# Kernel tuning notes

Measured on AMD Instinct MI355X. Metric: run time of the kernel, lower is better.

The kernel has to match this reference:

```python
import jax, jax.numpy as jnp
import numpy as np

B, H, S, D = 2, 16, 2048, 64

def setup_inputs() -> dict:
    key = jax.random.key(0)
    kq, kk, kv = jax.random.split(key, 3)
    q = jax.random.normal(kq, (B, H, S, D), dtype=jnp.float32)
    k = jax.random.normal(kk, (B, H, S, D), dtype=jnp.float32)
    v = jax.random.normal(kv, (B, H, S, D), dtype=jnp.float32)
    # causal mask: True where position j > i (future tokens are masked)
    mask = jnp.triu(jnp.ones((S, S), dtype=bool), k=1)[None, None, :, :]
    return {"q": q, "k": k, "v": v, "mask": mask}

def reference(q, k, v, mask) -> jnp.ndarray:
    # scaled dot-product attention with additive -1e4 mask bias
    scale = 1.0 / jnp.sqrt(jnp.asarray(q.shape[-1], q.dtype))
    scores = jnp.einsum('bhqd,bhkd->bhqk', q, k) * scale  # [B,H,S,S]
    scores = scores + mask.astype(scores.dtype) * jnp.asarray(-10000.0, scores.dtype)
    probs = jax.nn.softmax(scores, axis=-1)
    # dropout is identity in eval mode
    return jnp.einsum('bhqk,bhkd->bhqd', probs, v)
```

## Files before the change

### kernel.cpp

```cpp
#include <hip/hip_runtime.h>

typedef __bf16 bf16_t;
typedef bf16_t bf16x8 __attribute__((ext_vector_type(8)));
typedef bf16_t bf16x4 __attribute__((ext_vector_type(4)));
typedef float  floatx4 __attribute__((ext_vector_type(4)));

constexpr int Sq = 2048, Dq = 64;
constexpr int BQ = 64, BK = 64;
constexpr int NQT = Sq / BQ;
constexpr int STR = 72;
constexpr float SCALE_LOG2E = 0.125f * 1.44269504088896340736f;

__global__ __launch_bounds__(256, 2) void flash_attn_kernel(
    const float* __restrict__ Q, const float* __restrict__ K,
    const float* __restrict__ V, float* __restrict__ O)
{
    __shared__ bf16_t QPs[BQ][STR];
    __shared__ bf16_t Ks[BK][STR];
    __shared__ bf16_t VTs[Dq][STR];

    const int tid  = threadIdx.x;
    const int wave = tid >> 6;
    const int lane = tid & 63;
    const int quad = lane >> 4;
    const int l16  = lane & 15;

    const int id = blockIdx.x;
    const int bh = (id & 7) + ((id >> 7) << 3);
    const int pr = (id >> 3) & 15;
    const long base = (long)bh * Sq * Dq;

    const int r0 = tid >> 4;
    const int c4 = (tid & 15) * 4;
    const int h  = lane >> 3;
    const int jw = wave * 16;

    for (int half = 0; half < 2; ++half) {
        const int qt = half ? (NQT - 1 - pr) : pr;

        __syncthreads();
        #pragma unroll
        for (int p = 0; p < 4; ++p) {
            const int row = p * 16 + r0;
            const float4 qv = *(const float4*)&Q[base + (long)(qt * BQ + row) * Dq + c4];
            bf16x4 w;
            w[0] = (bf16_t)(qv.x * SCALE_LOG2E); w[1] = (bf16_t)(qv.y * SCALE_LOG2E);
            w[2] = (bf16_t)(qv.z * SCALE_LOG2E); w[3] = (bf16_t)(qv.w * SCALE_LOG2E);
            *(bf16x4*)&QPs[row][c4] = w;
        }
        __syncthreads();

        bf16x8 aq0, aq1;
        {
            const int qrow = wave * 16 + l16;
            aq0 = *(const bf16x8*)&QPs[qrow][quad * 8];
            aq1 = *(const bf16x8*)&QPs[qrow][32 + quad * 8];
        }

        float l_lane = 0.f;
        floatx4 o_acc[4];
        #pragma unroll
        for (int i = 0; i < 4; ++i) o_acc[i] = floatx4{0.f, 0.f, 0.f, 0.f};

        float4 kf[4];
        float  vf[4][4];
        #pragma unroll
        for (int p = 0; p < 4; ++p) {
            kf[p] = *(const float4*)&K[base + (long)(p * 16 + r0) * Dq + c4];
            const int j0 = jw + 4 * ((p + h) & 3);
            #pragma unroll
            for (int r = 0; r < 4; ++r)
                vf[p][r] = V[base + (long)(j0 + r) * Dq + lane];
        }

        for (int kt = 0; kt <= qt; ++kt) {
            __syncthreads();

            #pragma unroll
            for (int p = 0; p < 4; ++p) {
                bf16x4 w;
                w[0] = (bf16_t)kf[p].x; w[1] = (bf16_t)kf[p].y;
                w[2] = (bf16_t)kf[p].z; w[3] = (bf16_t)kf[p].w;
                *(bf16x4*)&Ks[p * 16 + r0][c4] = w;
                bf16x4 vw;
                vw[0] = (bf16_t)vf[p][0]; vw[1] = (bf16_t)vf[p][1];
                vw[2] = (bf16_t)vf[p][2]; vw[3] = (bf16_t)vf[p][3];
                *(bf16x4*)&VTs[lane][jw + 4 * ((p + h) & 3)] = vw;
            }
            __syncthreads();

            {
                const int kn = (kt < qt) ? (kt + 1) : qt;
                const long kb = base + (long)kn * BK * Dq;
                #pragma unroll
                for (int p = 0; p < 4; ++p) {
                    kf[p] = *(const float4*)&K[kb + (long)(p * 16 + r0) * Dq + c4];
                    const int j0 = jw + 4 * ((p + h) & 3);
                    #pragma unroll
                    for (int r = 0; r < 4; ++r)
                        vf[p][r] = V[kb + (long)(j0 + r) * Dq + lane];
                }
            }

            floatx4 acc[4];
            #pragma unroll
            for (int t = 0; t < 4; ++t) {
                acc[t] = floatx4{0.f, 0.f, 0.f, 0.f};
                const int krow = t * 16 + l16;
                bf16x8 ak0 = *(const bf16x8*)&Ks[krow][quad * 8];
                bf16x8 ak1 = *(const bf16x8*)&Ks[krow][32 + quad * 8];
                acc[t] = __builtin_amdgcn_mfma_f32_16x16x32_bf16(ak0, aq0, acc[t], 0, 0, 0);
                acc[t] = __builtin_amdgcn_mfma_f32_16x16x32_bf16(ak1, aq1, acc[t], 0, 0, 0);
            }

            if (kt == qt) {
                const int qr = wave * 16 + l16;
                #pragma unroll
                for (int t = 0; t < 4; ++t) {
                    #pragma unroll
                    for (int i = 0; i < 4; ++i) {
                        if (t * 16 + quad * 4 + i > qr) acc[t][i] = -1e30f;
                    }
                }
            }

            float l_add = 0.f;
            #pragma unroll
            for (int t = 0; t < 4; ++t) {
                #pragma unroll
                for (int i = 0; i < 4; ++i) {
                    acc[t][i] = __builtin_amdgcn_exp2f(acc[t][i]);
                    l_add += acc[t][i];
                }
            }
            l_lane += l_add;

            #pragma unroll
            for (int t = 0; t < 4; ++t) {
                bf16x4 pk;
                pk[0] = (bf16_t)acc[t][0]; pk[1] = (bf16_t)acc[t][1];
                pk[2] = (bf16_t)acc[t][2]; pk[3] = (bf16_t)acc[t][3];
                *(bf16x4*)&QPs[wave * 16 + l16][t * 16 + quad * 4] = pk;
            }

            bf16x8 ap0 = *(const bf16x8*)&QPs[wave * 16 + l16][quad * 8];
            bf16x8 ap1 = *(const bf16x8*)&QPs[wave * 16 + l16][32 + quad * 8];
            #pragma unroll
            for (int dt = 0; dt < 4; ++dt) {
                const int dcol = dt * 16 + l16;
                bf16x8 bv0 = *(const bf16x8*)&VTs[dcol][quad * 8];
                bf16x8 bv1 = *(const bf16x8*)&VTs[dcol][32 + quad * 8];
                o_acc[dt] = __builtin_amdgcn_mfma_f32_16x16x32_bf16(ap0, bv0, o_acc[dt], 0, 0, 0);
                o_acc[dt] = __builtin_amdgcn_mfma_f32_16x16x32_bf16(ap1, bv1, o_acc[dt], 0, 0, 0);
            }
        }

        float lsum = l_lane;
        lsum += __shfl_xor(lsum, 16);
        lsum += __shfl_xor(lsum, 32);
        #pragma unroll
        for (int i = 0; i < 4; ++i) {
            const float inv_l = 1.f / __shfl(lsum, quad * 4 + i, 16);
            const long row = (long)qt * BQ + wave * 16 + quad * 4 + i;
            #pragma unroll
            for (int dt = 0; dt < 4; ++dt) {
                O[base + row * Dq + dt * 16 + l16] = o_acc[dt][i] * inv_l;
            }
        }
    }
}

extern "C" void kernel_launch(void* const* d_in, const int* in_sizes, int n_in,
                              void* d_out, int out_size, void* d_ws, size_t ws_size,
                              hipStream_t stream)
{
    const float* q = (const float*)d_in[0];
    const float* k = (const float*)d_in[1];
    const float* v = (const float*)d_in[2];
    float* out = (float*)d_out;
    flash_attn_kernel<<<dim3(512, 1, 1), dim3(256, 1, 1), 0, stream>>>(q, k, v, out);
}
```

Before: 128.3 us.

## Double-buffer K/V shared tiles to drop one barrier per iteration

Splits the K and transposed-V shared tiles into two buffers. Each iteration writes the next tile into the spare buffer while computing on the current one, so only one barrier per iteration is needed instead of two. Register prefetch now runs two tiles ahead. Shared memory use grows by about 18 KB per block, which may limit occupancy at two blocks per CU.

```diff
diff --git a/kernel.cpp b/kernel.cpp
--- a/kernel.cpp
+++ b/kernel.cpp
@@ -16,8 +16,8 @@
     const float* __restrict__ V, float* __restrict__ O)
 {
     __shared__ bf16_t QPs[BQ][STR];
-    __shared__ bf16_t Ks[BK][STR];
-    __shared__ bf16_t VTs[Dq][STR];
+    __shared__ bf16_t Ks[2][BK][STR];
+    __shared__ bf16_t VTs[2][Dq][STR];
 
     const int tid  = threadIdx.x;
     const int wave = tid >> 6;
@@ -72,26 +72,49 @@
             for (int r = 0; r < 4; ++r)
                 vf[p][r] = V[base + (long)(j0 + r) * Dq + lane];
         }
+        #pragma unroll
+        for (int p = 0; p < 4; ++p) {
+            bf16x4 w;
+            w[0] = (bf16_t)kf[p].x; w[1] = (bf16_t)kf[p].y;
+            w[2] = (bf16_t)kf[p].z; w[3] = (bf16_t)kf[p].w;
+            *(bf16x4*)&Ks[0][p * 16 + r0][c4] = w;
+            bf16x4 vw;
+            vw[0] = (bf16_t)vf[p][0]; vw[1] = (bf16_t)vf[p][1];
+            vw[2] = (bf16_t)vf[p][2]; vw[3] = (bf16_t)vf[p][3];
+            *(bf16x4*)&VTs[0][lane][jw + 4 * ((p + h) & 3)] = vw;
+        }
+        {
+            const int kn = (qt > 0) ? 1 : 0;
+            const long kb = base + (long)kn * BK * Dq;
+            #pragma unroll
+            for (int p = 0; p < 4; ++p) {
+                kf[p] = *(const float4*)&K[kb + (long)(p * 16 + r0) * Dq + c4];
+                const int j0 = jw + 4 * ((p + h) & 3);
+                #pragma unroll
+                for (int r = 0; r < 4; ++r)
+                    vf[p][r] = V[kb + (long)(j0 + r) * Dq + lane];
+            }
+        }
+        __syncthreads();
 
         for (int kt = 0; kt <= qt; ++kt) {
-            __syncthreads();
-
-            #pragma unroll
-            for (int p = 0; p < 4; ++p) {
-                bf16x4 w;
-                w[0] = (bf16_t)kf[p].x; w[1] = (bf16_t)kf[p].y;
-                w[2] = (bf16_t)kf[p].z; w[3] = (bf16_t)kf[p].w;
-                *(bf16x4*)&Ks[p * 16 + r0][c4] = w;
-                bf16x4 vw;
-                vw[0] = (bf16_t)vf[p][0]; vw[1] = (bf16_t)vf[p][1];
-                vw[2] = (bf16_t)vf[p][2]; vw[3] = (bf16_t)vf[p][3];
-                *(bf16x4*)&VTs[lane][jw + 4 * ((p + h) & 3)] = vw;
-            }
-            __syncthreads();
-
-            {
-                const int kn = (kt < qt) ? (kt + 1) : qt;
-                const long kb = base + (long)kn * BK * Dq;
+            const int cur = kt & 1;
+
+            if (kt < qt) {
+                #pragma unroll
+                for (int p = 0; p < 4; ++p) {
+                    bf16x4 w;
+                    w[0] = (bf16_t)kf[p].x; w[1] = (bf16_t)kf[p].y;
+                    w[2] = (bf16_t)kf[p].z; w[3] = (bf16_t)kf[p].w;
+                    *(bf16x4*)&Ks[cur ^ 1][p * 16 + r0][c4] = w;
+                    bf16x4 vw;
+                    vw[0] = (bf16_t)vf[p][0]; vw[1] = (bf16_t)vf[p][1];
+                    vw[2] = (bf16_t)vf[p][2]; vw[3] = (bf16_t)vf[p][3];
+                    *(bf16x4*)&VTs[cur ^ 1][lane][jw + 4 * ((p + h) & 3)] = vw;
+                }
+            }
+            if (kt + 1 < qt) {
+                const long kb = base + (long)(kt + 2) * BK * Dq;
                 #pragma unroll
                 for (int p = 0; p < 4; ++p) {
                     kf[p] = *(const float4*)&K[kb + (long)(p * 16 + r0) * Dq + c4];
@@ -107,8 +130,8 @@
             for (int t = 0; t < 4; ++t) {
                 acc[t] = floatx4{0.f, 0.f, 0.f, 0.f};
                 const int krow = t * 16 + l16;
-                bf16x8 ak0 = *(const bf16x8*)&Ks[krow][quad * 8];
-                bf16x8 ak1 = *(const bf16x8*)&Ks[krow][32 + quad * 8];
+                bf16x8 ak0 = *(const bf16x8*)&Ks[cur][krow][quad * 8];
+                bf16x8 ak1 = *(const bf16x8*)&Ks[cur][krow][32 + quad * 8];
                 acc[t] = __builtin_amdgcn_mfma_f32_16x16x32_bf16(ak0, aq0, acc[t], 0, 0, 0);
                 acc[t] = __builtin_amdgcn_mfma_f32_16x16x32_bf16(ak1, aq1, acc[t], 0, 0, 0);
             }
@@ -148,11 +171,13 @@
             #pragma unroll
             for (int dt = 0; dt < 4; ++dt) {
                 const int dcol = dt * 16 + l16;
-                bf16x8 bv0 = *(const bf16x8*)&VTs[dcol][quad * 8];
-                bf16x8 bv1 = *(const bf16x8*)&VTs[dcol][32 + quad * 8];
+                bf16x8 bv0 = *(const bf16x8*)&VTs[cur][dcol][quad * 8];
+                bf16x8 bv1 = *(const bf16x8*)&VTs[cur][dcol][32 + quad * 8];
                 o_acc[dt] = __builtin_amdgcn_mfma_f32_16x16x32_bf16(ap0, bv0, o_acc[dt], 0, 0, 0);
                 o_acc[dt] = __builtin_amdgcn_mfma_f32_16x16x32_bf16(ap1, bv1, o_acc[dt], 0, 0, 0);
             }
+
+            __syncthreads();
         }
 
         float lsum = l_lane;
```

Result: slower. 134.2 us (+4.6%).

## Enlarge query tile to 128 rows per block, drop paired-tile scheduling

Applied to the files above, without the earlier changes.

The query tile grows from 64 to 128 rows, so each wave computes two 16-row query sub-tiles against every staged K/V tile. This halves K/V global loads, bf16 conversions and LDS staging per query row. The old scheme, where each block processed a light and a heavy 64-row tile for causal balance, is replaced by a single 128-row tile per block, with block-index remapping that interleaves ascending and descending tile order. Blocks now do very different amounts of causal work (2 to 32 key tiles), so load imbalance and a longer critical path are a risk.

```diff
diff --git a/kernel.cpp b/kernel.cpp
--- a/kernel.cpp
+++ b/kernel.cpp
@@ -6,7 +6,7 @@
 typedef float  floatx4 __attribute__((ext_vector_type(4)));
 
 constexpr int Sq = 2048, Dq = 64;
-constexpr int BQ = 64, BK = 64;
+constexpr int BQ = 128, BK = 64;
 constexpr int NQT = Sq / BQ;
 constexpr int STR = 72;
 constexpr float SCALE_LOG2E = 0.125f * 1.44269504088896340736f;
@@ -25,9 +25,12 @@
     const int quad = lane >> 4;
     const int l16  = lane & 15;
 
-    const int id = blockIdx.x;
-    const int bh = (id & 7) + ((id >> 7) << 3);
-    const int pr = (id >> 3) & 15;
+    const int b  = blockIdx.x;
+    const int x  = b & 255;
+    const int bh = (x & 7) | (((x >> 7) & 1) << 3) | (((b >> 8) & 1) << 4);
+    const int qidx = (x >> 3) & 15;
+    const int qt = (b >> 8) ? (NQT - 1 - qidx) : qidx;
+    const int ktmax = 2 * qt + 1;
     const long base = (long)bh * Sq * Dq;
 
     const int r0 = tid >> 4;
@@ -35,136 +38,157 @@
     const int h  = lane >> 3;
     const int jw = wave * 16;
 
-    for (int half = 0; half < 2; ++half) {
-        const int qt = half ? (NQT - 1 - pr) : pr;
-
+    #pragma unroll
+    for (int p = 0; p < 8; ++p) {
+        const int row = p * 16 + r0;
+        const float4 qv = *(const float4*)&Q[base + (long)(qt * BQ + row) * Dq + c4];
+        bf16x4 w;
+        w[0] = (bf16_t)(qv.x * SCALE_LOG2E); w[1] = (bf16_t)(qv.y * SCALE_LOG2E);
+        w[2] = (bf16_t)(qv.z * SCALE_LOG2E); w[3] = (bf16_t)(qv.w * SCALE_LOG2E);
+        *(bf16x4*)&QPs[row][c4] = w;
+    }
+    __syncthreads();
+
+    bf16x8 aq[2][2];
+    #pragma unroll
+    for (int u = 0; u < 2; ++u) {
+        #pragma unroll
+        for (int hh = 0; hh < 2; ++hh)
+            aq[u][hh] = *(const bf16x8*)&QPs[32 * wave + u * 16 + l16][hh * 32 + quad * 8];
+    }
+
+    float l_lane[2] = {0.f, 0.f};
+    floatx4 o_acc[2][4];
+    #pragma unroll
+    for (int u = 0; u < 2; ++u)
+        #pragma unroll
+        for (int dt = 0; dt < 4; ++dt) o_acc[u][dt] = floatx4{0.f, 0.f, 0.f, 0.f};
+
+    float4 kf[4];
+    float  vf[4][4];
+    #pragma unroll
+    for (int p = 0; p < 4; ++p) {
+        kf[p] = *(const float4*)&K[base + (long)(p * 16 + r0) * Dq + c4];
+        const int j0 = jw + 4 * ((p + h) & 3);
+        #pragma unroll
+        for (int r = 0; r < 4; ++r)
+            vf[p][r] = V[base + (long)(j0 + r) * Dq + lane];
+    }
+
+    for (int kt = 0; kt <= ktmax; ++kt) {
         __syncthreads();
+
         #pragma unroll
         for (int p = 0; p < 4; ++p) {
-            const int row = p * 16 + r0;
-            const float4 qv = *(const float4*)&Q[base + (long)(qt * BQ + row) * Dq + c4];
             bf16x4 w;
-            w[0] = (bf16_t)(qv.x * SCALE_LOG2E); w[1] = (bf16_t)(qv.y * SCALE_LOG2E);
-            w[2] = (bf16_t)(qv.z * SCALE_LOG2E); w[3] = (bf16_t)(qv.w * SCALE_LOG2E);
-            *(bf16x4*)&QPs[row][c4] = w;
+            w[0] = (bf16_t)kf[p].x; w[1] = (bf16_t)kf[p].y;
+            w[2] = (bf16_t)kf[p].z; w[3] = (bf16_t)kf[p].w;
+            *(bf16x4*)&Ks[p * 16 + r0][c4] = w;
+            bf16x4 vw;
+            vw[0] = (bf16_t)vf[p][0]; vw[1] = (bf16_t)vf[p][1];
+            vw[2] = (bf16_t)vf[p][2]; vw[3] = (bf16_t)vf[p][3];
+            *(bf16x4*)&VTs[lane][jw + 4 * ((p + h) & 3)] = vw;
         }
         __syncthreads();
 
-        bf16x8 aq0, aq1;
         {
-            const int qrow = wave * 16 + l16;
-            aq0 = *(const bf16x8*)&QPs[qrow][quad * 8];
-            aq1 = *(const bf16x8*)&QPs[qrow][32 + quad * 8];
-        }
-
-        float l_lane = 0.f;
-        floatx4 o_acc[4];
-        #pragma unroll
-        for (int i = 0; i < 4; ++i) o_acc[i] = floatx4{0.f, 0.f, 0.f, 0.f};
-
-        float4 kf[4];
-        float  vf[4][4];
-        #pragma unroll
-        for (int p = 0; p < 4; ++p) {
-            kf[p] = *(const float4*)&K[base + (long)(p * 16 + r0) * Dq + c4];
-            const int j0 = jw + 4 * ((p + h) & 3);
-            #pragma unroll
-            for (int r = 0; r < 4; ++r)
-                vf[p][r] = V[base + (long)(j0 + r) * Dq + lane];
-        }
-
-        for (int kt = 0; kt <= qt; ++kt) {
-            __syncthreads();
-
+            const int kn = (kt < ktmax) ? (kt + 1) : ktmax;
+            const long kb = base + (long)kn * BK * Dq;
             #pragma unroll
             for (int p = 0; p < 4; ++p) {
-                bf16x4 w;
-                w[0] = (bf16_t)kf[p].x; w[1] = (bf16_t)kf[p].y;
-                w[2] = (bf16_t)kf[p].z; w[3] = (bf16_t)kf[p].w;
-                *(bf16x4*)&Ks[p * 16 + r0][c4] = w;
-                bf16x4 vw;
-                vw[0] = (bf16_t)vf[p][0]; vw[1] = (bf16_t)vf[p][1];
-                vw[2] = (bf16_t)vf[p][2]; vw[3] = (bf16_t)vf[p][3];
-                *(bf16x4*)&VTs[lane][jw + 4 * ((p + h) & 3)] = vw;
-            }
-            __syncthreads();
-
-            {
-                const int kn = (kt < qt) ? (kt + 1) : qt;
-                const long kb = base + (long)kn * BK * Dq;
+                kf[p] = *(const float4*)&K[kb + (long)(p * 16 + r0) * Dq + c4];
+                const int j0 = jw + 4 * ((p + h) & 3);
                 #pragma unroll
-                for (int p = 0; p < 4; ++p) {
-                    kf[p] = *(const float4*)&K[kb + (long)(p * 16 + r0) * Dq + c4];
-                    const int j0 = jw + 4 * ((p + h) & 3);
-                    #pragma unroll
-                    for (int r = 0; r < 4; ++r)
-                        vf[p][r] = V[kb + (long)(j0 + r) * Dq + lane];
-                }
-            }
-
-            floatx4 acc[4];
-            #pragma unroll
-            for (int t = 0; t < 4; ++t) {
-                acc[t] = floatx4{0.f, 0.f, 0.f, 0.f};
-                const int krow = t * 16 + l16;
-                bf16x8 ak0 = *(const bf16x8*)&Ks[krow][quad * 8];
-                bf16x8 ak1 = *(const bf16x8*)&Ks[krow][32 + quad * 8];
-                acc[t] = __builtin_amdgcn_mfma_f32_16x16x32_bf16(ak0, aq0, acc[t], 0, 0, 0);
-                acc[t] = __builtin_amdgcn_mfma_f32_16x16x32_bf16(ak1, aq1, acc[t], 0, 0, 0);
-            }
-
-            if (kt == qt) {
-                const int qr = wave * 16 + l16;
+                for (int r = 0; r < 4; ++r)
+                    vf[p][r] = V[kb + (long)(j0 + r) * Dq + lane];
+            }
+        }
+
+        floatx4 acc[4][2];
+        #pragma unroll
+        for (int t = 0; t < 4; ++t) {
+            const int krow = t * 16 + l16;
+            bf16x8 ak0 = *(const bf16x8*)&Ks[krow][quad * 8];
+            bf16x8 ak1 = *(const bf16x8*)&Ks[krow][32 + quad * 8];
+            #pragma unroll
+            for (int u = 0; u < 2; ++u) {
+                acc[t][u] = floatx4{0.f, 0.f, 0.f, 0.f};
+                acc[t][u] = __builtin_amdgcn_mfma_f32_16x16x32_bf16(ak0, aq[u][0], acc[t][u], 0, 0, 0);
+                acc[t][u] = __builtin_amdgcn_mfma_f32_16x16x32_bf16(ak1, aq[u][1], acc[t][u], 0, 0, 0);
+            }
+        }
+
+        if (kt >= 2 * qt) {
+            #pragma unroll
+            for (int u = 0; u < 2; ++u) {
+                const int qr = qt * BQ + 32 * wave + u * 16 + l16;
                 #pragma unroll
                 for (int t = 0; t < 4; ++t) {
                     #pragma unroll
                     for (int i = 0; i < 4; ++i) {
-                        if (t * 16 + quad * 4 + i > qr) acc[t][i] = -1e30f;
+                        if (kt * BK + t * 16 + quad * 4 + i > qr) acc[t][u][i] = -1e30f;
                     }
                 }
             }
-
+        }
+
+        #pragma unroll
+        for (int u = 0; u < 2; ++u) {
             float l_add = 0.f;
             #pragma unroll
             for (int t = 0; t < 4; ++t) {
                 #pragma unroll
                 for (int i = 0; i < 4; ++i) {
-                    acc[t][i] = __builtin_amdgcn_exp2f(acc[t][i]);
-                    l_add += acc[t][i];
+                    acc[t][u][i] = __builtin_amdgcn_exp2f(acc[t][u][i]);
+                    l_add += acc[t][u][i];
                 }
             }
-            l_lane += l_add;
-
+            l_lane[u] += l_add;
+        }
+
+        #pragma unroll
+        for (int u = 0; u < 2; ++u) {
             #pragma unroll
             for (int t = 0; t < 4; ++t) {
                 bf16x4 pk;
-                pk[0] = (bf16_t)acc[t][0]; pk[1] = (bf16_t)acc[t][1];
-                pk[2] = (bf16_t)acc[t][2]; pk[3] = (bf16_t)acc[t][3];
-                *(bf16x4*)&QPs[wave * 16 + l16][t * 16 + quad * 4] = pk;
-            }
-
-            bf16x8 ap0 = *(const bf16x8*)&QPs[wave * 16 + l16][quad * 8];
-            bf16x8 ap1 = *(const bf16x8*)&QPs[wave * 16 + l16][32 + quad * 8];
-            #pragma unroll
-            for (int dt = 0; dt < 4; ++dt) {
-                const int dcol = dt * 16 + l16;
-                bf16x8 bv0 = *(const bf16x8*)&VTs[dcol][quad * 8];
-                bf16x8 bv1 = *(const bf16x8*)&VTs[dcol][32 + quad * 8];
-                o_acc[dt] = __builtin_amdgcn_mfma_f32_16x16x32_bf16(ap0, bv0, o_acc[dt], 0, 0, 0);
-                o_acc[dt] = __builtin_amdgcn_mfma_f32_16x16x32_bf16(ap1, bv1, o_acc[dt], 0, 0, 0);
-            }
-        }
-
-        float lsum = l_lane;
+                pk[0] = (bf16_t)acc[t][u][0]; pk[1] = (bf16_t)acc[t][u][1];
+                pk[2] = (bf16_t)acc[t][u][2]; pk[3] = (bf16_t)acc[t][u][3];
+                *(bf16x4*)&QPs[32 * wave + u * 16 + l16][t * 16 + quad * 4] = pk;
+            }
+        }
+
+        bf16x8 ap[2][2];
+        #pragma unroll
+        for (int u = 0; u < 2; ++u) {
+            #pragma unroll
+            for (int hh = 0; hh < 2; ++hh)
+                ap[u][hh] = *(const bf16x8*)&QPs[32 * wave + u * 16 + l16][hh * 32 + quad * 8];
+        }
+        #pragma unroll
+        for (int dt = 0; dt < 4; ++dt) {
+            const int dcol = dt * 16 + l16;
+            bf16x8 bv0 = *(const bf16x8*)&VTs[dcol][quad * 8];
+            bf16x8 bv1 = *(const bf16x8*)&VTs[dcol][32 + quad * 8];
+            #pragma unroll
+            for (int u = 0; u < 2; ++u) {
+                o_acc[u][dt] = __builtin_amdgcn_mfma_f32_16x16x32_bf16(ap[u][0], bv0, o_acc[u][dt], 0, 0, 0);
+                o_acc[u][dt] = __builtin_amdgcn_mfma_f32_16x16x32_bf16(ap[u][1], bv1, o_acc[u][dt], 0, 0, 0);
+            }
+        }
+    }
+
+    #pragma unroll
+    for (int u = 0; u < 2; ++u) {
+        float lsum = l_lane[u];
         lsum += __shfl_xor(lsum, 16);
         lsum += __shfl_xor(lsum, 32);
         #pragma unroll
         for (int i = 0; i < 4; ++i) {
             const float inv_l = 1.f / __shfl(lsum, quad * 4 + i, 16);
-            const long row = (long)qt * BQ + wave * 16 + quad * 4 + i;
+            const long row = (long)qt * BQ + 32 * wave + u * 16 + quad * 4 + i;
             #pragma unroll
             for (int dt = 0; dt < 4; ++dt) {
-                O[base + row * Dq + dt * 16 + l16] = o_acc[dt][i] * inv_l;
+                O[base + row * Dq + dt * 16 + l16] = o_acc[u][dt][i] * inv_l;
             }
         }
     }
```

New measurement: 135.1 us. +5.3%, slower.
